# Performance work log

Measured on AMD Instinct MI355X. Metric: run time of the kernel, lower is better.

The kernel has to match this reference:

```python
import jax, jax.numpy as jnp
import numpy as np

MAX_CLUSTERS = 5
CLUSTER_SIZE_MAX = 3
K_HOP = 2
TAU = 1.0  # epoch=0 -> tau_init * decay^0 = 1.0
NEG = -1e9


def _logits(x, ctx, W1, b1, W2, b2):
    # x: [B,N,D], ctx: [B,H] -> logits [B,N] (selection_mlp, dropout=eval/identity)
    B, N, _ = x.shape
    h = jnp.concatenate([x, jnp.broadcast_to(ctx[:, None, :], (B, N, ctx.shape[-1]))], axis=-1)
    h = jax.nn.relu(h @ W1.T + b1)
    return (h @ W2.T + b2)[..., 0]


def _select(logits, cand, key):
    # Hard Gumbel-Softmax argmax over candidate nodes; zeros row if no candidates.
    any_c = cand.any(axis=-1, keepdims=True)
    ml = jnp.where(cand, logits, NEG)
    u = jax.random.uniform(key, logits.shape, dtype=logits.dtype)
    g = -jnp.log(-jnp.log(u + 1e-8) + 1e-8)
    idx = jnp.argmax((ml + g) / TAU, axis=-1)
    oh = jax.nn.one_hot(idx, logits.shape[-1], dtype=logits.dtype)
    return oh * any_c.astype(logits.dtype)


def _gru(seq, h0, Wih, Whh, bih, bhh):
    # torch nn.GRU single layer, batch_first; seq: [B,T,D], h0: [B,H] -> final hidden [B,H]
    def cell(h, xt):
        gi = xt @ Wih.T + bih
        gh = h @ Whh.T + bhh
        ir, iz, inn = jnp.split(gi, 3, axis=-1)
        hr, hz, hn = jnp.split(gh, 3, axis=-1)
        r = jax.nn.sigmoid(ir + hr)
        z = jax.nn.sigmoid(iz + hz)
        n = jnp.tanh(inn + r * hn)
        return (1.0 - z) * n + z * h, None
    h, _ = jax.lax.scan(cell, h0, jnp.swapaxes(seq, 0, 1))
    return h


def reference(x, adj, mask, W1, b1, W2, b2, Wc, bc, Wih, Whh, bih, bhh):
    B, N, D = x.shape
    key = jax.random.key(42)
    avail = mask.astype(bool)
    ctx = x.mean(axis=1) @ Wc.T + bc          # context_init  [B,H]
    h_gru = jnp.zeros_like(ctx)               # context_hidden
    assign = jnp.zeros((B, N, MAX_CLUSTERS), x.dtype)
    embs, hist = [], []
    for c in range(MAX_CLUSTERS):
        # logits are identical for every selection within this cluster (same x, same context)
        logits = _logits(x, ctx, W1, b1, W2, b2)  # [B,N]
        # seed selection (torch uses .item() -> selection is a constant index; no grad path)
        seed = jax.lax.stop_gradient(_select(logits, avail, jax.random.fold_in(key, 2 * c)))
        avail = avail & ~(seed > 0.5)
        # k-hop BFS from seed via adjacency matvecs
        reach = seed > 0.5
        cur = seed
        for _ in range(K_HOP):
            nb = jnp.einsum('bn,bnm->bm', cur, adj) > 0
            new = nb & ~reach
            reach = reach | nb
            cur = new.astype(x.dtype)
        member = seed
        for a in range(CLUSTER_SIZE_MAX - 1):
            cand = avail & reach
            sel = jax.lax.stop_gradient(_select(logits, cand, jax.random.fold_in(key, 2 * c + 1000 + a)))
            avail = avail & ~(sel > 0.5)
            member = member + sel
        assign = assign.at[:, :, c].set(member)
        cnt = member.sum(axis=-1, keepdims=True)
        emb = jnp.einsum('bn,bnd->bd', member, x) / jnp.maximum(cnt, 1.0)  # mean of member feats; 0 if empty
        embs.append(emb)
        hist.append(emb)
        # torch re-runs the GRU over the FULL cluster history each iteration, starting
        # from the previously updated hidden state (faithful to the original code)
        h_gru = _gru(jnp.stack(hist, axis=1), h_gru, Wih, Whh, bih, bhh)
        ctx = h_gru
    cluster_features = jnp.stack(embs, axis=1)               # [B,S,D]
    S = MAX_CLUSTERS
    cluster_adj = jnp.ones((B, S, S), x.dtype) - jnp.eye(S, dtype=x.dtype)[None]
    return cluster_features, cluster_adj, assign


def setup_inputs() -> dict:
    key = jax.random.key(0)
    ks = jax.random.split(key, 10)
    B, N, D, H = 16, 2048, 128, 64
    x = jax.random.normal(ks[0], (B, N, D), dtype=jnp.float32)
    # sparse symmetric binary adjacency, ~16 neighbors per node
    a = (jax.random.uniform(ks[1], (B, N, N)) < 0.004).astype(jnp.float32)
    adj = jnp.clip(a + jnp.swapaxes(a, 1, 2), 0.0, 1.0)
    adj = adj * (1.0 - jnp.eye(N, dtype=jnp.float32)[None])
    mask = jnp.ones((B, N), dtype=jnp.int32)
    s = 0.05
    return {
        'x': x, 'adj': adj, 'mask': mask,
        'W1': jax.random.normal(ks[2], (H, D + H)) * s, 'b1': jnp.zeros((H,)),
        'W2': jax.random.normal(ks[3], (1, H)) * s, 'b2': jnp.zeros((1,)),
        'Wc': jax.random.normal(ks[4], (H, D)) * s, 'bc': jnp.zeros((H,)),
        'Wih': jax.random.normal(ks[5], (3 * H, D)) * s,
        'Whh': jax.random.normal(ks[6], (3 * H, H)) * s,
        'bih': jnp.zeros((3 * H,)), 'bhh': jnp.zeros((3 * H,)),
    }
```

## Files before the change

### kernel.cpp

```cpp
#include <hip/hip_runtime.h>
#include <cfloat>
#include <cmath>

#define NB 2048
#define BB 16
#define DD 128
#define HH 64
#define MAXC 5
#define CSMAX 3
#define NT 1024

__device__ __forceinline__ unsigned rotl32(unsigned v, int d) {
  return (v << d) | (v >> (32 - d));
}

__device__ __forceinline__ void tf2x32(unsigned k0, unsigned k1, unsigned x0, unsigned x1,
                                       unsigned& o0, unsigned& o1) {
  unsigned ks2 = k0 ^ k1 ^ 0x1BD11BDAu;
  x0 += k0; x1 += k1;
#define RND(r) { x0 += x1; x1 = rotl32(x1, r); x1 ^= x0; }
  RND(13) RND(15) RND(26) RND(6)   x0 += k1;  x1 += ks2 + 1u;
  RND(17) RND(29) RND(16) RND(24)  x0 += ks2; x1 += k0 + 2u;
  RND(13) RND(15) RND(26) RND(6)   x0 += k0;  x1 += k1 + 3u;
  RND(17) RND(29) RND(16) RND(24)  x0 += k1;  x1 += ks2 + 4u;
  RND(13) RND(15) RND(26) RND(6)   x0 += ks2; x1 += k0 + 5u;
#undef RND
  o0 = x0; o1 = x1;
}

__device__ __forceinline__ float gumbel_for(unsigned k0, unsigned k1, unsigned idx) {
  unsigned o0, o1;
  tf2x32(k0, k1, 0u, idx, o0, o1);
  unsigned bits = o0 ^ o1;
  float u = __uint_as_float((bits >> 9) | 0x3f800000u) - 1.0f;
  float uu = u + 1e-8f;
  return -logf(-logf(uu) + 1e-8f);
}

__global__ __launch_bounds__(NT) void gvp_prep(
    const float* __restrict__ x, const float* __restrict__ W1,
    float* __restrict__ P, float* __restrict__ partial, float* __restrict__ gumb) {
  __shared__ __align__(16) float s_W1[HH][DD + 4];
  __shared__ float sp[8][DD];
  const int bid = blockIdx.x, tid = threadIdx.x;

  if (bid < 128) {
    for (int i = tid; i < HH * (DD / 4); i += NT) {
      int r = i >> 5, q = i & 31;
      *(float4*)&s_W1[r][q * 4] = *(const float4*)(W1 + (size_t)r * (DD + HH) + q * 4);
    }
    __syncthreads();
    const int jg = tid & 15, ng = tid >> 4;
    const int j0 = jg * 4;
    const size_t n0 = (size_t)bid * 256 + ng * 4;
    const float4* x4 = (const float4*)x;
    float acc[4][4];
#pragma unroll
    for (int i = 0; i < 4; i++)
#pragma unroll
      for (int q = 0; q < 4; q++) acc[i][q] = 0.f;
    for (int kq = 0; kq < 32; kq++) {
      float4 xv[4], wv[4];
#pragma unroll
      for (int i = 0; i < 4; i++) xv[i] = x4[(n0 + i) * 32 + kq];
#pragma unroll
      for (int q = 0; q < 4; q++) wv[q] = *(const float4*)&s_W1[j0 + q][kq * 4];
#pragma unroll
      for (int i = 0; i < 4; i++)
#pragma unroll
        for (int q = 0; q < 4; q++)
          acc[i][q] += xv[i].x * wv[q].x + xv[i].y * wv[q].y +
                       xv[i].z * wv[q].z + xv[i].w * wv[q].w;
    }
#pragma unroll
    for (int i = 0; i < 4; i++)
#pragma unroll
      for (int q = 0; q < 4; q++)
        P[(n0 + i) * HH + j0 + q] = acc[i][q];
  } else if (bid < 384) {
    const int bm = bid - 128;
    const int b = bm >> 4, chunk = bm & 15;
    const int d = tid & (DD - 1), part = tid >> 7;
    float acc = 0.f;
    const int base = chunk * 128 + part;
#pragma unroll
    for (int k = 0; k < 16; k++)
      acc += x[((size_t)b * NB + base + k * 8) * DD + d];
    sp[part][d] = acc;
    __syncthreads();
    if (tid < DD) {
      float m = 0.f;
#pragma unroll
      for (int p = 0; p < 8; p++) m += sp[p][tid];
      partial[((size_t)b * 16 + chunk) * DD + tid] = m;
    }
  } else {
    const int bg = bid - 384;
    const int base = (bg * NT + tid) * 4;
#pragma unroll
    for (int i = 0; i < 4; i++) {
      int idx = base + i;
      int sel = idx >> 15;
      int rem = idx & 32767;
      int c = sel / 3, s = sel - 3 * c;
      unsigned data = (s == 0) ? (unsigned)(2 * c) : (unsigned)(2 * c + 1000 + (s - 1));
      unsigned k0, k1;
      tf2x32(0u, 42u, 0u, data, k0, k1);
      gumb[idx] = gumbel_for(k0, k1, (unsigned)rem);
    }
  }
}

__global__ __launch_bounds__(NT, 4) void gvp_main(
    const float* __restrict__ x, const float* __restrict__ adj, const int* __restrict__ mask,
    const float* __restrict__ W1, const float* __restrict__ b1,
    const float* __restrict__ W2, const float* __restrict__ b2,
    const float* __restrict__ Wc, const float* __restrict__ bc,
    const float* __restrict__ Wih, const float* __restrict__ Whh,
    const float* __restrict__ bih, const float* __restrict__ bhh,
    const float* __restrict__ P, const float* __restrict__ partial,
    const float* __restrict__ gumb,
    float* __restrict__ out_feat, float* __restrict__ out_adjm, float* __restrict__ out_assign) {
  const int b = blockIdx.x;
  const int tid = threadIdx.x;

  __shared__ __align__(16) float s_logits[NB];
  __shared__ __align__(16) float s_gumb[2][NB];
  __shared__ unsigned char s_avail[NB], s_reach[NB], s_assignB[NB];
  __shared__ short s_list[128];
  __shared__ int s_cnt;
  __shared__ unsigned long long s_key[CSMAX];
  __shared__ __align__(16) float s_ctx[HH], s_q[HH];
  __shared__ __align__(16) float s_h[2][HH];
  __shared__ __align__(16) float s_hist[MAXC][DD];
  __shared__ __align__(16) float s_giAll[MAXC][3 * HH];
  __shared__ __align__(16) float s_Whh[3 * HH][HH + 4];
  __shared__ __align__(16) float s_W1c[HH][HH + 4];
  __shared__ __align__(16) float s_W2[HH];
  __shared__ float s_bhh[3 * HH], s_b1[HH];
  __shared__ __align__(16) float s_mean[DD];
  __shared__ float s_b2v;

  const size_t xb = (size_t)b * NB * DD;
  const float4* adj4 = (const float4*)(adj + (size_t)b * NB * NB);
  const float4* P4 = (const float4*)(P + (size_t)b * NB * HH);

  auto scanReduce = [&](float bv, int bi, int slot) {
#pragma unroll
    for (int off = 32; off; off >>= 1) {
      float ov = __shfl_down(bv, off);
      int oi = __shfl_down(bi, off);
      if (ov > bv || (ov == bv && oi < bi)) { bv = ov; bi = oi; }
    }
    if ((tid & 63) == 0 && bi < NB) {
      unsigned u = __float_as_uint(bv);
      u = (u & 0x80000000u) ? ~u : (u | 0x80000000u);
      unsigned long long key = ((unsigned long long)u << 32) | (unsigned)(~bi);
      atomicMax(&s_key[slot], key);
    }
  };
  auto decodeIdx = [](unsigned long long k) -> int {
    return k ? (int)(unsigned)(~(unsigned)k) : -1;
  };

  for (int i = tid; i < 3 * HH * (HH / 4); i += NT) {
    int r = i >> 4, q = i & 15;
    *(float4*)&s_Whh[r][q * 4] = *(const float4*)(Whh + (size_t)r * HH + q * 4);
  }
  {
    int r = tid >> 4, q = tid & 15;
    *(float4*)&s_W1c[r][q * 4] = *(const float4*)(W1 + (size_t)r * (DD + HH) + DD + q * 4);
  }
  if (tid < 3 * HH) s_bhh[tid] = bhh[tid];
  if (tid < HH) { s_W2[tid] = W2[tid]; s_b1[tid] = b1[tid]; s_h[0][tid] = 0.f; }
  if (tid == 0) s_b2v = b2[0];
#pragma unroll
  for (int r = 0; r < 2; r++) {
    int n = tid + r * NT;
    s_avail[n] = (mask[b * NB + n] != 0) ? 1 : 0;
    s_assignB[n] = 0;
  }
  if (tid < DD) {
    float m = 0.f;
#pragma unroll
    for (int k = 0; k < 16; k++) m += partial[((size_t)b * 16 + k) * DD + tid];
    s_mean[tid] = m * (1.0f / NB);
  }
  __syncthreads();
  if (tid < 4 * HH) {
    int row = tid >> 2, g = tid & 3;
    const float4* wr = (const float4*)(Wc + (size_t)row * DD) + g * 8;
    const float4* m4 = (const float4*)s_mean + g * 8;
    float s = 0.f;
#pragma unroll
    for (int i = 0; i < 8; i++) {
      float4 w = wr[i], m = m4[i];
      s += w.x * m.x + w.y * m.y + w.z * m.z + w.w * m.w;
    }
    s += __shfl_xor(s, 1);
    s += __shfl_xor(s, 2);
    if (g == 0) s_ctx[row] = s + bc[row];
  }
  __syncthreads();

  int hp = 0;

  for (int c = 0; c < MAXC; c++) {
    const float* g0p = gumb + ((size_t)(c * 3) * BB + b) * NB;
    const float4* g12 = (const float4*)(gumb + ((size_t)(c * 3 + 1 + (tid >> 9)) * BB + b) * NB);
    float4 gst = g12[tid & 511];
    const int n0 = tid, n1 = tid + NT;
    float gs0 = g0p[n0], gs1 = g0p[n1];
    ((float4*)s_gumb)[tid] = gst;
    if (tid < 4 * HH) {
      int row = tid >> 2, g = tid & 3;
      const float4* wr = (const float4*)&s_W1c[row][0] + g * 4;
      const float4* c4 = (const float4*)s_ctx + g * 4;
      float s = 0.f;
#pragma unroll
      for (int i = 0; i < 4; i++) {
        float4 w = wr[i], cc = c4[i];
        s += w.x * cc.x + w.y * cc.y + w.z * cc.z + w.w * cc.w;
      }
      s += __shfl_xor(s, 1);
      s += __shfl_xor(s, 2);
      if (g == 0) s_q[row] = s + s_b1[row];
    }
    if (tid < CSMAX) s_key[tid] = 0ull;
    if (tid == 0) s_cnt = 0;
    __syncthreads();

    {
      float l0 = s_b2v, l1 = s_b2v;
      const float4* p0 = P4 + (size_t)n0 * 16;
      const float4* p1 = P4 + (size_t)n1 * 16;
      const float4* q4 = (const float4*)s_q;
      const float4* w4 = (const float4*)s_W2;
#pragma unroll
      for (int qq = 0; qq < 16; qq += 4) {
        float4 A[4], Bv[4];
#pragma unroll
        for (int i = 0; i < 4; i++) { A[i] = p0[qq + i]; Bv[i] = p1[qq + i]; }
#pragma unroll
        for (int i = 0; i < 4; i++) {
          float4 qv = q4[qq + i], w = w4[qq + i];
          l0 += w.x * fmaxf(A[i].x + qv.x, 0.f) + w.y * fmaxf(A[i].y + qv.y, 0.f) +
                w.z * fmaxf(A[i].z + qv.z, 0.f) + w.w * fmaxf(A[i].w + qv.w, 0.f);
          l1 += w.x * fmaxf(Bv[i].x + qv.x, 0.f) + w.y * fmaxf(Bv[i].y + qv.y, 0.f) +
                w.z * fmaxf(Bv[i].z + qv.z, 0.f) + w.w * fmaxf(Bv[i].w + qv.w, 0.f);
        }
      }
      s_logits[n0] = l0;
      s_logits[n1] = l1;
      float bv = -FLT_MAX;
      int bi = NB;
      if (s_avail[n0]) { float y = l0 + gs0; if (y > bv) { bv = y; bi = n0; } }
      if (s_avail[n1]) { float y = l1 + gs1; if (y > bv || (y == bv && n1 < bi)) { bv = y; bi = n1; } }
      scanReduce(bv, bi, 0);
    }
    __syncthreads();

    const int seed = decodeIdx(s_key[0]);
    if (tid < 512) {
      if (seed >= 0) {
        float4 a = adj4[(size_t)seed * 512 + tid];
        int m = tid << 2;
        unsigned f0 = a.x > 0.f, f1 = a.y > 0.f, f2 = a.z > 0.f, f3 = a.w > 0.f;
        unsigned r = f0 | (f1 << 8) | (f2 << 16) | (f3 << 24);
        if ((seed >> 2) == tid) r |= 1u << ((seed & 3) * 8);
        ((unsigned*)s_reach)[tid] = r;
        if (f0 && m != seed)     { int p = atomicAdd(&s_cnt, 1); if (p < 128) s_list[p] = (short)m; }
        if (f1 && m + 1 != seed) { int p = atomicAdd(&s_cnt, 1); if (p < 128) s_list[p] = (short)(m + 1); }
        if (f2 && m + 2 != seed) { int p = atomicAdd(&s_cnt, 1); if (p < 128) s_list[p] = (short)(m + 2); }
        if (f3 && m + 3 != seed) { int p = atomicAdd(&s_cnt, 1); if (p < 128) s_list[p] = (short)(m + 3); }
      } else {
        ((unsigned*)s_reach)[tid] = 0u;
      }
    }
    __syncthreads();

    if (seed >= 0) {
      int cnt = min(s_cnt, 128);
      int m4 = tid & 511, rg = tid >> 9;
      bool a0 = false, a1 = false, a2 = false, a3 = false;
#pragma unroll
      for (int k = 0; k < 20; k++) {
        int li = rg + 2 * k;
        if (li < cnt) {
          int n = s_list[li];
          float4 a = adj4[(size_t)n * 512 + m4];
          a0 |= a.x > 0.f; a1 |= a.y > 0.f; a2 |= a.z > 0.f; a3 |= a.w > 0.f;
        }
      }
      for (int li = rg + 40; li < cnt; li += 2) {
        int n = s_list[li];
        float4 a = adj4[(size_t)n * 512 + m4];
        a0 |= a.x > 0.f; a1 |= a.y > 0.f; a2 |= a.z > 0.f; a3 |= a.w > 0.f;
      }
      int m = m4 << 2;
      if (a0) s_reach[m] = 1;
      if (a1) s_reach[m + 1] = 1;
      if (a2) s_reach[m + 2] = 1;
      if (a3) s_reach[m + 3] = 1;
    }
    __syncthreads();

    {
      float bv = -FLT_MAX;
      int bi = NB;
#pragma unroll
      for (int r = 0; r < 2; r++) {
        int n = tid + r * NT;
        if (s_avail[n] && s_reach[n] && n != seed) {
          float y = s_logits[n] + s_gumb[0][n];
          if (y > bv || (y == bv && n < bi)) { bv = y; bi = n; }
        }
      }
      scanReduce(bv, bi, 1);
    }
    __syncthreads();

    const int w1i = decodeIdx(s_key[1]);
    {
      float bv = -FLT_MAX;
      int bi = NB;
#pragma unroll
      for (int r = 0; r < 2; r++) {
        int n = tid + r * NT;
        if (s_avail[n] && s_reach[n] && n != seed && n != w1i) {
          float y = s_logits[n] + s_gumb[1][n];
          if (y > bv || (y == bv && n < bi)) { bv = y; bi = n; }
        }
      }
      scanReduce(bv, bi, 2);
    }
    __syncthreads();

    const int w2i = decodeIdx(s_key[2]);
    {
      int mc = (seed >= 0) + (w1i >= 0) + (w2i >= 0);
      if (tid < DD) {
        float acc = 0.f;
        if (seed >= 0) acc += x[xb + (size_t)seed * DD + tid];
        if (w1i >= 0) acc += x[xb + (size_t)w1i * DD + tid];
        if (w2i >= 0) acc += x[xb + (size_t)w2i * DD + tid];
        float e = acc / fmaxf((float)mc, 1.0f);
        s_hist[c][tid] = e;
        out_feat[((size_t)b * MAXC + c) * DD + tid] = e;
      } else if (tid >= 128 && tid < 128 + CSMAX) {
        int idx = (tid == 128) ? seed : (tid == 129 ? w1i : w2i);
        if (idx >= 0) { s_avail[idx] = 0; s_assignB[idx] |= (unsigned char)(1 << c); }
      }
    }
    __syncthreads();

    if (tid < 4 * 3 * HH) {
      int row = tid >> 2, g = tid & 3;
      const float4* wr = (const float4*)(Wih + (size_t)row * DD) + g * 8;
      const float4* h4 = (const float4*)s_hist[c] + g * 8;
      float s = 0.f;
#pragma unroll
      for (int i = 0; i < 8; i++) {
        float4 w = wr[i], hh = h4[i];
        s += w.x * hh.x + w.y * hh.y + w.z * hh.z + w.w * hh.w;
      }
      s += __shfl_xor(s, 1);
      s += __shfl_xor(s, 2);
      if (g == 0) s_giAll[c][row] = s + bih[row];
    }
    __syncthreads();

    for (int t0 = 0; t0 <= c; t0++) {
      if (tid < 4 * HH) {
        int row = tid >> 2, g = tid & 3;
        const float4* h4 = (const float4*)s_h[hp] + g * 4;
        float4 hv[4];
#pragma unroll
        for (int i = 0; i < 4; i++) hv[i] = h4[i];
        const float4* wr = (const float4*)&s_Whh[row][0] + g * 4;
        const float4* wz = (const float4*)&s_Whh[HH + row][0] + g * 4;
        const float4* wn = (const float4*)&s_Whh[2 * HH + row][0] + g * 4;
        float sr = 0.f, sz = 0.f, sn = 0.f;
#pragma unroll
        for (int i = 0; i < 4; i++) {
          float4 a = wr[i], bz = wz[i], cn = wn[i], h = hv[i];
          sr += a.x * h.x + a.y * h.y + a.z * h.z + a.w * h.w;
          sz += bz.x * h.x + bz.y * h.y + bz.z * h.z + bz.w * h.w;
          sn += cn.x * h.x + cn.y * h.y + cn.z * h.z + cn.w * h.w;
        }
        sr += __shfl_xor(sr, 1); sr += __shfl_xor(sr, 2);
        sz += __shfl_xor(sz, 1); sz += __shfl_xor(sz, 2);
        sn += __shfl_xor(sn, 1); sn += __shfl_xor(sn, 2);
        if (g == 0) {
          float r = 1.f / (1.f + expf(-(s_giAll[t0][row] + sr + s_bhh[row])));
          float z = 1.f / (1.f + expf(-(s_giAll[t0][HH + row] + sz + s_bhh[HH + row])));
          float nn = tanhf(s_giAll[t0][2 * HH + row] + r * (sn + s_bhh[2 * HH + row]));
          float hn = (1.f - z) * nn + z * s_h[hp][row];
          s_h[hp ^ 1][row] = hn;
          if (t0 == c) s_ctx[row] = hn;
        }
      }
      hp ^= 1;
      __syncthreads();
    }
  }

#pragma unroll
  for (int r = 0; r < 2; r++) {
    int n = tid + r * NT;
    unsigned bits = s_assignB[n];
    size_t base = ((size_t)(b * NB + n)) * MAXC;
#pragma unroll
    for (int cc = 0; cc < MAXC; cc++)
      out_assign[base + cc] = (float)((bits >> cc) & 1u);
  }
  for (int i = tid; i < MAXC * MAXC; i += NT)
    out_adjm[(size_t)b * MAXC * MAXC + i] = ((i / MAXC) == (i % MAXC)) ? 0.f : 1.f;
}

extern "C" void kernel_launch(void* const* d_in, const int* in_sizes, int n_in,
                              void* d_out, int out_size, void* d_ws, size_t ws_size,
                              hipStream_t stream) {
  const float* x   = (const float*)d_in[0];
  const float* adj = (const float*)d_in[1];
  const int*   mask= (const int*)d_in[2];
  const float* W1  = (const float*)d_in[3];
  const float* b1  = (const float*)d_in[4];
  const float* W2  = (const float*)d_in[5];
  const float* b2  = (const float*)d_in[6];
  const float* Wc  = (const float*)d_in[7];
  const float* bc  = (const float*)d_in[8];
  const float* Wih = (const float*)d_in[9];
  const float* Whh = (const float*)d_in[10];
  const float* bih = (const float*)d_in[11];
  const float* bhh = (const float*)d_in[12];

  float* ws = (float*)d_ws;
  float* P       = ws;
  float* partial = P + (size_t)BB * NB * HH;
  float* gumb    = partial + (size_t)BB * 16 * DD;

  float* out = (float*)d_out;
  float* out_feat = out;
  float* out_adjm = out + (size_t)BB * MAXC * DD;
  float* out_assign = out_adjm + (size_t)BB * MAXC * MAXC;

  hipLaunchKernelGGL(gvp_prep, dim3(504), dim3(NT), 0, stream, x, W1, P, partial, gumb);
  hipLaunchKernelGGL(gvp_main, dim3(BB), dim3(NT), 0, stream,
                     x, adj, mask, W1, b1, W2, b2, Wc, bc, Wih, Whh, bih, bhh, P, partial, gumb,
                     out_feat, out_adjm, out_assign);
}
```

Baseline: 195.0 us.

## Split monolithic per-batch kernel into per-cluster launches with inline Gumbel noise

Replaces the single persistent 16-block main kernel with a chain of small kernels per cluster: logits plus seed selection, BFS plus a joint top-2 pick of both members, a GRU update, and a final assignment writer. Gumbel noise is now computed inline instead of being precomputed into a large buffer, and the two sequential member argmaxes are merged into one top-2 reduction. State is passed between launches through workspace. This adds about 16 launches, each still using only 16 blocks, and moves state through global memory, trading launch overhead for less serialized work inside one block.

```diff
diff --git a/kernel.cpp b/kernel.cpp
--- a/kernel.cpp
+++ b/kernel.cpp
@@ -7,8 +7,15 @@
 #define DD 128
 #define HH 64
 #define MAXC 5
-#define CSMAX 3
 #define NT 1024
+
+#define OFF_P 0
+#define OFF_PARTIAL (OFF_P + BB * NB * HH)
+#define OFF_LOGITS OFF_PARTIAL
+#define OFF_QV (OFF_PARTIAL + BB * 16 * DD)
+#define OFF_HRUN (OFF_QV + BB * HH)
+#define OFF_GI (OFF_HRUN + BB * HH)
+#define OFF_WIN (OFF_GI + BB * MAXC * 3 * HH)
 
 __device__ __forceinline__ unsigned rotl32(unsigned v, int d) {
   return (v << d) | (v >> (32 - d));
@@ -37,12 +44,22 @@
   return -logf(-logf(uu) + 1e-8f);
 }
 
+__device__ __forceinline__ unsigned long long packKey(float y, int n) {
+  unsigned u = __float_as_uint(y);
+  u = (u & 0x80000000u) ? ~u : (u | 0x80000000u);
+  return ((unsigned long long)u << 32) | (unsigned)(~(unsigned)n);
+}
+__device__ __forceinline__ int decodeKey(unsigned long long k) {
+  return k ? (int)(~(unsigned)k) : -1;
+}
+
 __global__ __launch_bounds__(NT) void gvp_prep(
-    const float* __restrict__ x, const float* __restrict__ W1,
-    float* __restrict__ P, float* __restrict__ partial, float* __restrict__ gumb) {
+    const float* __restrict__ x, const float* __restrict__ W1, float* __restrict__ ws) {
   __shared__ __align__(16) float s_W1[HH][DD + 4];
   __shared__ float sp[8][DD];
   const int bid = blockIdx.x, tid = threadIdx.x;
+  float* P = ws + OFF_P;
+  float* partial = ws + OFF_PARTIAL;
 
   if (bid < 128) {
     for (int i = tid; i < HH * (DD / 4); i += NT) {
@@ -77,7 +94,7 @@
 #pragma unroll
       for (int q = 0; q < 4; q++)
         P[(n0 + i) * HH + j0 + q] = acc[i][q];
-  } else if (bid < 384) {
+  } else {
     const int bm = bid - 128;
     const int b = bm >> 4, chunk = bm & 15;
     const int d = tid & (DD - 1), part = tid >> 7;
@@ -94,328 +111,372 @@
       for (int p = 0; p < 8; p++) m += sp[p][tid];
       partial[((size_t)b * 16 + chunk) * DD + tid] = m;
     }
-  } else {
-    const int bg = bid - 384;
-    const int base = (bg * NT + tid) * 4;
+  }
+}
+
+__global__ __launch_bounds__(256) void gvp_init(
+    const float* __restrict__ Wc, const float* __restrict__ bc,
+    const float* __restrict__ W1, const float* __restrict__ b1, float* __restrict__ ws) {
+  __shared__ __align__(16) float s_mean[DD], s_ctx[HH];
+  __shared__ __align__(16) float s_W1c[HH][HH + 4];
+  const int b = blockIdx.x, tid = threadIdx.x;
+  for (int i = tid; i < HH * 16; i += 256) {
+    int r = i >> 4, q = i & 15;
+    *(float4*)&s_W1c[r][q * 4] = *(const float4*)(W1 + (size_t)r * (DD + HH) + DD + q * 4);
+  }
+  if (tid < DD) {
+    float m = 0.f;
+#pragma unroll
+    for (int k = 0; k < 16; k++) m += ws[OFF_PARTIAL + ((size_t)b * 16 + k) * DD + tid];
+    s_mean[tid] = m * (1.0f / NB);
+  }
+  __syncthreads();
+  {
+    int row = tid >> 2, g = tid & 3;
+    const float4* wr = (const float4*)(Wc + (size_t)row * DD) + g * 8;
+    const float4* m4 = (const float4*)s_mean + g * 8;
+    float s = 0.f;
+#pragma unroll
+    for (int i = 0; i < 8; i++) {
+      float4 w = wr[i], m = m4[i];
+      s += w.x * m.x + w.y * m.y + w.z * m.z + w.w * m.w;
+    }
+    s += __shfl_xor(s, 1);
+    s += __shfl_xor(s, 2);
+    if (g == 0) s_ctx[row] = s + bc[row];
+  }
+  __syncthreads();
+  {
+    int row = tid >> 2, g = tid & 3;
+    const float4* wr = (const float4*)&s_W1c[row][0] + g * 4;
+    const float4* c4 = (const float4*)s_ctx + g * 4;
+    float s = 0.f;
 #pragma unroll
     for (int i = 0; i < 4; i++) {
-      int idx = base + i;
-      int sel = idx >> 15;
-      int rem = idx & 32767;
-      int c = sel / 3, s = sel - 3 * c;
-      unsigned data = (s == 0) ? (unsigned)(2 * c) : (unsigned)(2 * c + 1000 + (s - 1));
-      unsigned k0, k1;
-      tf2x32(0u, 42u, 0u, data, k0, k1);
-      gumb[idx] = gumbel_for(k0, k1, (unsigned)rem);
-    }
-  }
-}
-
-__global__ __launch_bounds__(NT, 4) void gvp_main(
+      float4 w = wr[i], cc = c4[i];
+      s += w.x * cc.x + w.y * cc.y + w.z * cc.z + w.w * cc.w;
+    }
+    s += __shfl_xor(s, 1);
+    s += __shfl_xor(s, 2);
+    if (g == 0) ws[OFF_QV + b * HH + row] = s + b1[row];
+  }
+  if (tid < HH) ws[OFF_HRUN + b * HH + tid] = 0.f;
+}
+
+__global__ __launch_bounds__(NT) void gvp_selA(
+    const int* __restrict__ mask, const float* __restrict__ W2, const float* __restrict__ b2,
+    float* __restrict__ ws, int c) {
+  __shared__ __align__(16) float s_q[HH], s_W2[HH];
+  __shared__ int s_win[16];
+  __shared__ unsigned long long s_key0;
+  const int b = blockIdx.x, tid = threadIdx.x;
+  const int n0 = tid, n1 = tid + NT;
+  int* winners = (int*)(ws + OFF_WIN) + b * 16;
+
+  if (tid == 0) s_key0 = 0ull;
+  if (tid < HH) s_q[tid] = ws[OFF_QV + b * HH + tid];
+  else if (tid < 2 * HH) s_W2[tid - HH] = W2[tid - HH];
+  else if (tid < 2 * HH + 16) {
+    int i = tid - 2 * HH;
+    s_win[i] = (i < 3 * c) ? winners[i] : -1;
+  }
+  __syncthreads();
+
+  const float4* P4 = (const float4*)(ws + OFF_P) + (size_t)b * NB * 16;
+  const float4* q4 = (const float4*)s_q;
+  const float4* w4 = (const float4*)s_W2;
+  const float4* p0 = P4 + (size_t)n0 * 16;
+  const float4* p1 = P4 + (size_t)n1 * 16;
+  float l0 = b2[0], l1 = l0;
+#pragma unroll
+  for (int i = 0; i < 16; i++) {
+    float4 pa = p0[i], pb = p1[i], qv = q4[i], w = w4[i];
+    l0 += w.x * fmaxf(pa.x + qv.x, 0.f) + w.y * fmaxf(pa.y + qv.y, 0.f) +
+          w.z * fmaxf(pa.z + qv.z, 0.f) + w.w * fmaxf(pa.w + qv.w, 0.f);
+    l1 += w.x * fmaxf(pb.x + qv.x, 0.f) + w.y * fmaxf(pb.y + qv.y, 0.f) +
+          w.z * fmaxf(pb.z + qv.z, 0.f) + w.w * fmaxf(pb.w + qv.w, 0.f);
+  }
+  ws[OFF_LOGITS + (size_t)b * NB + n0] = l0;
+  ws[OFF_LOGITS + (size_t)b * NB + n1] = l1;
+
+  unsigned k0, k1;
+  tf2x32(0u, 42u, 0u, (unsigned)(2 * c), k0, k1);
+  bool a0 = mask[b * NB + n0] != 0, a1 = mask[b * NB + n1] != 0;
+  for (int i = 0; i < 3 * c; i++) {
+    int w = s_win[i];
+    a0 &= (n0 != w);
+    a1 &= (n1 != w);
+  }
+  float bv = -FLT_MAX;
+  int bi = NB;
+  if (a0) { float y = l0 + gumbel_for(k0, k1, (unsigned)(b * NB + n0)); if (y > bv) { bv = y; bi = n0; } }
+  if (a1) { float y = l1 + gumbel_for(k0, k1, (unsigned)(b * NB + n1)); if (y > bv) { bv = y; bi = n1; } }
+#pragma unroll
+  for (int off = 32; off; off >>= 1) {
+    float ov = __shfl_down(bv, off);
+    int oi = __shfl_down(bi, off);
+    if (ov > bv || (ov == bv && oi < bi)) { bv = ov; bi = oi; }
+  }
+  if ((tid & 63) == 0 && bi < NB) atomicMax(&s_key0, packKey(bv, bi));
+  __syncthreads();
+  if (tid == 0) winners[3 * c] = decodeKey(s_key0);
+}
+
+__global__ __launch_bounds__(NT) void gvp_selB(
     const float* __restrict__ x, const float* __restrict__ adj, const int* __restrict__ mask,
-    const float* __restrict__ W1, const float* __restrict__ b1,
-    const float* __restrict__ W2, const float* __restrict__ b2,
-    const float* __restrict__ Wc, const float* __restrict__ bc,
-    const float* __restrict__ Wih, const float* __restrict__ Whh,
-    const float* __restrict__ bih, const float* __restrict__ bhh,
-    const float* __restrict__ P, const float* __restrict__ partial,
-    const float* __restrict__ gumb,
-    float* __restrict__ out_feat, float* __restrict__ out_adjm, float* __restrict__ out_assign) {
-  const int b = blockIdx.x;
-  const int tid = threadIdx.x;
-
+    const float* __restrict__ Wih, const float* __restrict__ bih,
+    float* __restrict__ ws, float* __restrict__ out_feat, int c) {
   __shared__ __align__(16) float s_logits[NB];
-  __shared__ __align__(16) float s_gumb[2][NB];
-  __shared__ unsigned char s_avail[NB], s_reach[NB], s_assignB[NB];
+  __shared__ unsigned char s_avail[NB], s_reach[NB];
   __shared__ short s_list[128];
   __shared__ int s_cnt;
-  __shared__ unsigned long long s_key[CSMAX];
-  __shared__ __align__(16) float s_ctx[HH], s_q[HH];
-  __shared__ __align__(16) float s_h[2][HH];
-  __shared__ __align__(16) float s_hist[MAXC][DD];
-  __shared__ __align__(16) float s_giAll[MAXC][3 * HH];
-  __shared__ __align__(16) float s_Whh[3 * HH][HH + 4];
-  __shared__ __align__(16) float s_W1c[HH][HH + 4];
-  __shared__ __align__(16) float s_W2[HH];
-  __shared__ float s_bhh[3 * HH], s_b1[HH];
-  __shared__ __align__(16) float s_mean[DD];
-  __shared__ float s_b2v;
-
+  __shared__ unsigned long long s_key1;
+  __shared__ unsigned long long s_top2[16][2];
+  __shared__ int s_win[16];
+  const int b = blockIdx.x, tid = threadIdx.x, wid = tid >> 6;
+  const int n0 = tid, n1 = tid + NT;
+  int* winners = (int*)(ws + OFF_WIN) + b * 16;
+  const float4* adj4 = (const float4*)(adj + (size_t)b * NB * NB);
   const size_t xb = (size_t)b * NB * DD;
-  const float4* adj4 = (const float4*)(adj + (size_t)b * NB * NB);
-  const float4* P4 = (const float4*)(P + (size_t)b * NB * HH);
-
-  auto scanReduce = [&](float bv, int bi, int slot) {
+
+  if (tid == 0) { s_cnt = 0; s_key1 = 0ull; }
+  if (tid >= 32 && tid < 64) s_top2[(tid - 32) >> 1][(tid - 32) & 1] = 0ull;
+  if (tid >= 64 && tid < 80) {
+    int i = tid - 64;
+    s_win[i] = (i <= 3 * c) ? winners[i] : -1;
+  }
+  s_logits[n0] = ws[OFF_LOGITS + (size_t)b * NB + n0];
+  s_logits[n1] = ws[OFF_LOGITS + (size_t)b * NB + n1];
+  s_avail[n0] = (mask[b * NB + n0] != 0) ? 1 : 0;
+  s_avail[n1] = (mask[b * NB + n1] != 0) ? 1 : 0;
+  __syncthreads();
+
+  const int seed = s_win[3 * c];
+  if (tid < 512) {
+    if (seed >= 0) {
+      float4 a = adj4[(size_t)seed * 512 + tid];
+      int m = tid << 2;
+      unsigned f0 = a.x > 0.f, f1 = a.y > 0.f, f2 = a.z > 0.f, f3 = a.w > 0.f;
+      unsigned r = f0 | (f1 << 8) | (f2 << 16) | (f3 << 24);
+      if ((seed >> 2) == tid) r |= 1u << ((seed & 3) * 8);
+      ((unsigned*)s_reach)[tid] = r;
+      if (f0 && m != seed)     { int p = atomicAdd(&s_cnt, 1); if (p < 128) s_list[p] = (short)m; }
+      if (f1 && m + 1 != seed) { int p = atomicAdd(&s_cnt, 1); if (p < 128) s_list[p] = (short)(m + 1); }
+      if (f2 && m + 2 != seed) { int p = atomicAdd(&s_cnt, 1); if (p < 128) s_list[p] = (short)(m + 2); }
+      if (f3 && m + 3 != seed) { int p = atomicAdd(&s_cnt, 1); if (p < 128) s_list[p] = (short)(m + 3); }
+    } else {
+      ((unsigned*)s_reach)[tid] = 0u;
+    }
+  }
+  unsigned k10, k11, k20, k21;
+  tf2x32(0u, 42u, 0u, (unsigned)(2 * c + 1000), k10, k11);
+  tf2x32(0u, 42u, 0u, (unsigned)(2 * c + 1001), k20, k21);
+  float g1a = gumbel_for(k10, k11, (unsigned)(b * NB + n0));
+  float g1b = gumbel_for(k10, k11, (unsigned)(b * NB + n1));
+  float g2a = gumbel_for(k20, k21, (unsigned)(b * NB + n0));
+  float g2b = gumbel_for(k20, k21, (unsigned)(b * NB + n1));
+  __syncthreads();
+
+  if (seed >= 0) {
+    int cnt = min(s_cnt, 128);
+    int m4 = tid & 511, rg = tid >> 9;
+    bool a0 = false, a1 = false, a2 = false, a3 = false;
+#pragma unroll
+    for (int k = 0; k < 20; k++) {
+      int li = rg + 2 * k;
+      if (li < cnt) {
+        int n = s_list[li];
+        float4 a = adj4[(size_t)n * 512 + m4];
+        a0 |= a.x > 0.f; a1 |= a.y > 0.f; a2 |= a.z > 0.f; a3 |= a.w > 0.f;
+      }
+    }
+    for (int li = rg + 40; li < cnt; li += 2) {
+      int n = s_list[li];
+      float4 a = adj4[(size_t)n * 512 + m4];
+      a0 |= a.x > 0.f; a1 |= a.y > 0.f; a2 |= a.z > 0.f; a3 |= a.w > 0.f;
+    }
+    int m = m4 << 2;
+    if (a0) s_reach[m] = 1;
+    if (a1) s_reach[m + 1] = 1;
+    if (a2) s_reach[m + 2] = 1;
+    if (a3) s_reach[m + 3] = 1;
+  }
+  __syncthreads();
+
+  {
+    bool c0 = s_avail[n0] && s_reach[n0];
+    bool c1 = s_avail[n1] && s_reach[n1];
+    for (int i = 0; i <= 3 * c; i++) {
+      int w = s_win[i];
+      c0 &= (n0 != w);
+      c1 &= (n1 != w);
+    }
+    float bv = -FLT_MAX;
+    int bi = NB;
+    if (c0) { float y = s_logits[n0] + g1a; if (y > bv) { bv = y; bi = n0; } }
+    if (c1) { float y = s_logits[n1] + g1b; if (y > bv || (y == bv && n1 < bi)) { bv = y; bi = n1; } }
+    unsigned long long ka = c0 ? packKey(s_logits[n0] + g2a, n0) : 0ull;
+    unsigned long long kb = c1 ? packKey(s_logits[n1] + g2b, n1) : 0ull;
+    unsigned long long t1 = ka > kb ? ka : kb, t2 = ka > kb ? kb : ka;
 #pragma unroll
     for (int off = 32; off; off >>= 1) {
       float ov = __shfl_down(bv, off);
       int oi = __shfl_down(bi, off);
       if (ov > bv || (ov == bv && oi < bi)) { bv = ov; bi = oi; }
-    }
-    if ((tid & 63) == 0 && bi < NB) {
-      unsigned u = __float_as_uint(bv);
-      u = (u & 0x80000000u) ? ~u : (u | 0x80000000u);
-      unsigned long long key = ((unsigned long long)u << 32) | (unsigned)(~bi);
-      atomicMax(&s_key[slot], key);
-    }
-  };
-  auto decodeIdx = [](unsigned long long k) -> int {
-    return k ? (int)(unsigned)(~(unsigned)k) : -1;
-  };
-
-  for (int i = tid; i < 3 * HH * (HH / 4); i += NT) {
-    int r = i >> 4, q = i & 15;
-    *(float4*)&s_Whh[r][q * 4] = *(const float4*)(Whh + (size_t)r * HH + q * 4);
-  }
+      unsigned long long o1 = __shfl_down(t1, off);
+      unsigned long long o2 = __shfl_down(t2, off);
+      unsigned long long lo = t1 < o1 ? t1 : o1;
+      unsigned long long hi2 = t2 > o2 ? t2 : o2;
+      t1 = t1 > o1 ? t1 : o1;
+      t2 = lo > hi2 ? lo : hi2;
+    }
+    if ((tid & 63) == 0) {
+      if (bi < NB) atomicMax(&s_key1, packKey(bv, bi));
+      s_top2[wid][0] = t1;
+      s_top2[wid][1] = t2;
+    }
+  }
+  __syncthreads();
+
   {
-    int r = tid >> 4, q = tid & 15;
-    *(float4*)&s_W1c[r][q * 4] = *(const float4*)(W1 + (size_t)r * (DD + HH) + DD + q * 4);
-  }
-  if (tid < 3 * HH) s_bhh[tid] = bhh[tid];
-  if (tid < HH) { s_W2[tid] = W2[tid]; s_b1[tid] = b1[tid]; s_h[0][tid] = 0.f; }
-  if (tid == 0) s_b2v = b2[0];
-#pragma unroll
-  for (int r = 0; r < 2; r++) {
-    int n = tid + r * NT;
-    s_avail[n] = (mask[b * NB + n] != 0) ? 1 : 0;
-    s_assignB[n] = 0;
-  }
-  if (tid < DD) {
-    float m = 0.f;
-#pragma unroll
-    for (int k = 0; k < 16; k++) m += partial[((size_t)b * 16 + k) * DD + tid];
-    s_mean[tid] = m * (1.0f / NB);
-  }
-  __syncthreads();
-  if (tid < 4 * HH) {
-    int row = tid >> 2, g = tid & 3;
-    const float4* wr = (const float4*)(Wc + (size_t)row * DD) + g * 8;
-    const float4* m4 = (const float4*)s_mean + g * 8;
-    float s = 0.f;
-#pragma unroll
-    for (int i = 0; i < 8; i++) {
-      float4 w = wr[i], m = m4[i];
-      s += w.x * m.x + w.y * m.y + w.z * m.z + w.w * m.w;
-    }
-    s += __shfl_xor(s, 1);
-    s += __shfl_xor(s, 2);
-    if (g == 0) s_ctx[row] = s + bc[row];
-  }
-  __syncthreads();
-
-  int hp = 0;
-
-  for (int c = 0; c < MAXC; c++) {
-    const float* g0p = gumb + ((size_t)(c * 3) * BB + b) * NB;
-    const float4* g12 = (const float4*)(gumb + ((size_t)(c * 3 + 1 + (tid >> 9)) * BB + b) * NB);
-    float4 gst = g12[tid & 511];
-    const int n0 = tid, n1 = tid + NT;
-    float gs0 = g0p[n0], gs1 = g0p[n1];
-    ((float4*)s_gumb)[tid] = gst;
-    if (tid < 4 * HH) {
+    int w1 = decodeKey(s_key1);
+    unsigned long long t1 = 0ull, t2 = 0ull;
+#pragma unroll
+    for (int i = 0; i < 16; i++) {
+      unsigned long long k = s_top2[i][0];
+      if (k > t1) { t2 = t1; t1 = k; } else if (k > t2) t2 = k;
+      k = s_top2[i][1];
+      if (k > t1) { t2 = t1; t1 = k; } else if (k > t2) t2 = k;
+    }
+    int i1 = decodeKey(t1);
+    int w2 = (i1 == w1) ? decodeKey(t2) : i1;
+    int mc = (seed >= 0) + (w1 >= 0) + (w2 >= 0);
+    float invmc = 1.0f / fmaxf((float)mc, 1.0f);
+
+    if (tid < 768) {
       int row = tid >> 2, g = tid & 3;
-      const float4* wr = (const float4*)&s_W1c[row][0] + g * 4;
-      const float4* c4 = (const float4*)s_ctx + g * 4;
+      const float4* wr = (const float4*)(Wih + (size_t)row * DD) + g * 8;
+      const float4* x0 = (seed >= 0) ? (const float4*)(x + xb + (size_t)seed * DD) + g * 8 : nullptr;
+      const float4* x1 = (w1 >= 0) ? (const float4*)(x + xb + (size_t)w1 * DD) + g * 8 : nullptr;
+      const float4* x2 = (w2 >= 0) ? (const float4*)(x + xb + (size_t)w2 * DD) + g * 8 : nullptr;
       float s = 0.f;
 #pragma unroll
-      for (int i = 0; i < 4; i++) {
-        float4 w = wr[i], cc = c4[i];
-        s += w.x * cc.x + w.y * cc.y + w.z * cc.z + w.w * cc.w;
+      for (int i = 0; i < 8; i++) {
+        float4 w = wr[i];
+        float sx = 0.f, sy = 0.f, sz = 0.f, sw = 0.f;
+        if (x0) { float4 v = x0[i]; sx += v.x; sy += v.y; sz += v.z; sw += v.w; }
+        if (x1) { float4 v = x1[i]; sx += v.x; sy += v.y; sz += v.z; sw += v.w; }
+        if (x2) { float4 v = x2[i]; sx += v.x; sy += v.y; sz += v.z; sw += v.w; }
+        s += w.x * sx + w.y * sy + w.z * sz + w.w * sw;
       }
       s += __shfl_xor(s, 1);
       s += __shfl_xor(s, 2);
-      if (g == 0) s_q[row] = s + s_b1[row];
-    }
-    if (tid < CSMAX) s_key[tid] = 0ull;
-    if (tid == 0) s_cnt = 0;
+      if (g == 0) ws[OFF_GI + ((size_t)b * MAXC + c) * 3 * HH + row] = s * invmc + bih[row];
+    } else if (tid < 768 + DD) {
+      int d = tid - 768;
+      float acc = 0.f;
+      if (seed >= 0) acc += x[xb + (size_t)seed * DD + d];
+      if (w1 >= 0) acc += x[xb + (size_t)w1 * DD + d];
+      if (w2 >= 0) acc += x[xb + (size_t)w2 * DD + d];
+      out_feat[((size_t)b * MAXC + c) * DD + d] = acc * invmc;
+    } else if (tid == 896) winners[3 * c + 1] = w1;
+    else if (tid == 897) winners[3 * c + 2] = w2;
+  }
+}
+
+__global__ __launch_bounds__(256) void gvp_gru(
+    const float* __restrict__ Whh, const float* __restrict__ bhh,
+    const float* __restrict__ W1, const float* __restrict__ b1,
+    float* __restrict__ ws, int c) {
+  __shared__ __align__(16) float s_Whh[3 * HH][HH + 4];
+  __shared__ __align__(16) float s_W1c[HH][HH + 4];
+  __shared__ __align__(16) float s_gi[MAXC][3 * HH];
+  __shared__ __align__(16) float s_h[2][HH];
+  __shared__ float s_bhh[3 * HH];
+  const int b = blockIdx.x, tid = threadIdx.x;
+
+  for (int i = tid; i < 3 * HH * 16; i += 256) {
+    int r = i >> 4, q = i & 15;
+    *(float4*)&s_Whh[r][q * 4] = *(const float4*)(Whh + (size_t)r * HH + q * 4);
+  }
+  for (int i = tid; i < HH * 16; i += 256) {
+    int r = i >> 4, q = i & 15;
+    *(float4*)&s_W1c[r][q * 4] = *(const float4*)(W1 + (size_t)r * (DD + HH) + DD + q * 4);
+  }
+  if (tid < 3 * HH) {
+    s_bhh[tid] = bhh[tid];
+    for (int t = 0; t <= c; t++)
+      s_gi[t][tid] = ws[OFF_GI + ((size_t)b * MAXC + t) * 3 * HH + tid];
+  }
+  if (tid < HH) s_h[0][tid] = ws[OFF_HRUN + b * HH + tid];
+  __syncthreads();
+
+  int hp = 0;
+  for (int t = 0; t <= c; t++) {
+    int row = tid >> 2, g = tid & 3;
+    const float4* h4 = (const float4*)s_h[hp] + g * 4;
+    float4 hv[4];
+#pragma unroll
+    for (int i = 0; i < 4; i++) hv[i] = h4[i];
+    const float4* wr = (const float4*)&s_Whh[row][0] + g * 4;
+    const float4* wz = (const float4*)&s_Whh[HH + row][0] + g * 4;
+    const float4* wn = (const float4*)&s_Whh[2 * HH + row][0] + g * 4;
+    float sr = 0.f, sz = 0.f, sn = 0.f;
+#pragma unroll
+    for (int i = 0; i < 4; i++) {
+      float4 a = wr[i], bz = wz[i], cn = wn[i], h = hv[i];
+      sr += a.x * h.x + a.y * h.y + a.z * h.z + a.w * h.w;
+      sz += bz.x * h.x + bz.y * h.y + bz.z * h.z + bz.w * h.w;
+      sn += cn.x * h.x + cn.y * h.y + cn.z * h.z + cn.w * h.w;
+    }
+    sr += __shfl_xor(sr, 1); sr += __shfl_xor(sr, 2);
+    sz += __shfl_xor(sz, 1); sz += __shfl_xor(sz, 2);
+    sn += __shfl_xor(sn, 1); sn += __shfl_xor(sn, 2);
+    if (g == 0) {
+      float r = 1.f / (1.f + expf(-(s_gi[t][row] + sr + s_bhh[row])));
+      float z = 1.f / (1.f + expf(-(s_gi[t][HH + row] + sz + s_bhh[HH + row])));
+      float nn = tanhf(s_gi[t][2 * HH + row] + r * (sn + s_bhh[2 * HH + row]));
+      s_h[hp ^ 1][row] = (1.f - z) * nn + z * s_h[hp][row];
+    }
+    hp ^= 1;
     __syncthreads();
-
-    {
-      float l0 = s_b2v, l1 = s_b2v;
-      const float4* p0 = P4 + (size_t)n0 * 16;
-      const float4* p1 = P4 + (size_t)n1 * 16;
-      const float4* q4 = (const float4*)s_q;
-      const float4* w4 = (const float4*)s_W2;
-#pragma unroll
-      for (int qq = 0; qq < 16; qq += 4) {
-        float4 A[4], Bv[4];
-#pragma unroll
-        for (int i = 0; i < 4; i++) { A[i] = p0[qq + i]; Bv[i] = p1[qq + i]; }
-#pragma unroll
-        for (int i = 0; i < 4; i++) {
-          float4 qv = q4[qq + i], w = w4[qq + i];
-          l0 += w.x * fmaxf(A[i].x + qv.x, 0.f) + w.y * fmaxf(A[i].y + qv.y, 0.f) +
-                w.z * fmaxf(A[i].z + qv.z, 0.f) + w.w * fmaxf(A[i].w + qv.w, 0.f);
-          l1 += w.x * fmaxf(Bv[i].x + qv.x, 0.f) + w.y * fmaxf(Bv[i].y + qv.y, 0.f) +
-                w.z * fmaxf(Bv[i].z + qv.z, 0.f) + w.w * fmaxf(Bv[i].w + qv.w, 0.f);
-        }
-      }
-      s_logits[n0] = l0;
-      s_logits[n1] = l1;
-      float bv = -FLT_MAX;
-      int bi = NB;
-      if (s_avail[n0]) { float y = l0 + gs0; if (y > bv) { bv = y; bi = n0; } }
-      if (s_avail[n1]) { float y = l1 + gs1; if (y > bv || (y == bv && n1 < bi)) { bv = y; bi = n1; } }
-      scanReduce(bv, bi, 0);
-    }
+  }
+  {
+    int row = tid >> 2, g = tid & 3;
+    const float4* wr = (const float4*)&s_W1c[row][0] + g * 4;
+    const float4* c4 = (const float4*)s_h[hp] + g * 4;
+    float s = 0.f;
+#pragma unroll
+    for (int i = 0; i < 4; i++) {
+      float4 w = wr[i], cc = c4[i];
+      s += w.x * cc.x + w.y * cc.y + w.z * cc.z + w.w * cc.w;
+    }
+    s += __shfl_xor(s, 1);
+    s += __shfl_xor(s, 2);
+    if (g == 0) ws[OFF_QV + b * HH + row] = s + b1[row];
+  }
+  if (tid < HH) ws[OFF_HRUN + b * HH + tid] = s_h[hp][tid];
+}
+
+__global__ __launch_bounds__(NT) void gvp_final(
+    const float* __restrict__ ws, float* __restrict__ out_adjm, float* __restrict__ out_assign) {
+  __shared__ int s_win[16];
+  const int tid = threadIdx.x;
+  if (blockIdx.x < 160) {
+    int b = blockIdx.x / 10;
+    const int* winners = (const int*)(ws + OFF_WIN) + b * 16;
+    if (tid < 16) s_win[tid] = (tid < 15) ? winners[tid] : -1;
     __syncthreads();
-
-    const int seed = decodeIdx(s_key[0]);
-    if (tid < 512) {
-      if (seed >= 0) {
-        float4 a = adj4[(size_t)seed * 512 + tid];
-        int m = tid << 2;
-        unsigned f0 = a.x > 0.f, f1 = a.y > 0.f, f2 = a.z > 0.f, f3 = a.w > 0.f;
-        unsigned r = f0 | (f1 << 8) | (f2 << 16) | (f3 << 24);
-        if ((seed >> 2) == tid) r |= 1u << ((seed & 3) * 8);
-        ((unsigned*)s_reach)[tid] = r;
-        if (f0 && m != seed)     { int p = atomicAdd(&s_cnt, 1); if (p < 128) s_list[p] = (short)m; }
-        if (f1 && m + 1 != seed) { int p = atomicAdd(&s_cnt, 1); if (p < 128) s_list[p] = (short)(m + 1); }
-        if (f2 && m + 2 != seed) { int p = atomicAdd(&s_cnt, 1); if (p < 128) s_list[p] = (short)(m + 2); }
-        if (f3 && m + 3 != seed) { int p = atomicAdd(&s_cnt, 1); if (p < 128) s_list[p] = (short)(m + 3); }
-      } else {
-        ((unsigned*)s_reach)[tid] = 0u;
-      }
-    }
-    __syncthreads();
-
-    if (seed >= 0) {
-      int cnt = min(s_cnt, 128);
-      int m4 = tid & 511, rg = tid >> 9;
-      bool a0 = false, a1 = false, a2 = false, a3 = false;
-#pragma unroll
-      for (int k = 0; k < 20; k++) {
-        int li = rg + 2 * k;
-        if (li < cnt) {
-          int n = s_list[li];
-          float4 a = adj4[(size_t)n * 512 + m4];
-          a0 |= a.x > 0.f; a1 |= a.y > 0.f; a2 |= a.z > 0.f; a3 |= a.w > 0.f;
-        }
-      }
-      for (int li = rg + 40; li < cnt; li += 2) {
-        int n = s_list[li];
-        float4 a = adj4[(size_t)n * 512 + m4];
-        a0 |= a.x > 0.f; a1 |= a.y > 0.f; a2 |= a.z > 0.f; a3 |= a.w > 0.f;
-      }
-      int m = m4 << 2;
-      if (a0) s_reach[m] = 1;
-      if (a1) s_reach[m + 1] = 1;
-      if (a2) s_reach[m + 2] = 1;
-      if (a3) s_reach[m + 3] = 1;
-    }
-    __syncthreads();
-
-    {
-      float bv = -FLT_MAX;
-      int bi = NB;
-#pragma unroll
-      for (int r = 0; r < 2; r++) {
-        int n = tid + r * NT;
-        if (s_avail[n] && s_reach[n] && n != seed) {
-          float y = s_logits[n] + s_gumb[0][n];
-          if (y > bv || (y == bv && n < bi)) { bv = y; bi = n; }
-        }
-      }
-      scanReduce(bv, bi, 1);
-    }
-    __syncthreads();
-
-    const int w1i = decodeIdx(s_key[1]);
-    {
-      float bv = -FLT_MAX;
-      int bi = NB;
-#pragma unroll
-      for (int r = 0; r < 2; r++) {
-        int n = tid + r * NT;
-        if (s_avail[n] && s_reach[n] && n != seed && n != w1i) {
-          float y = s_logits[n] + s_gumb[1][n];
-          if (y > bv || (y == bv && n < bi)) { bv = y; bi = n; }
-        }
-      }
-      scanReduce(bv, bi, 2);
-    }
-    __syncthreads();
-
-    const int w2i = decodeIdx(s_key[2]);
-    {
-      int mc = (seed >= 0) + (w1i >= 0) + (w2i >= 0);
-      if (tid < DD) {
-        float acc = 0.f;
-        if (seed >= 0) acc += x[xb + (size_t)seed * DD + tid];
-        if (w1i >= 0) acc += x[xb + (size_t)w1i * DD + tid];
-        if (w2i >= 0) acc += x[xb + (size_t)w2i * DD + tid];
-        float e = acc / fmaxf((float)mc, 1.0f);
-        s_hist[c][tid] = e;
-        out_feat[((size_t)b * MAXC + c) * DD + tid] = e;
-      } else if (tid >= 128 && tid < 128 + CSMAX) {
-        int idx = (tid == 128) ? seed : (tid == 129 ? w1i : w2i);
-        if (idx >= 0) { s_avail[idx] = 0; s_assignB[idx] |= (unsigned char)(1 << c); }
-      }
-    }
-    __syncthreads();
-
-    if (tid < 4 * 3 * HH) {
-      int row = tid >> 2, g = tid & 3;
-      const float4* wr = (const float4*)(Wih + (size_t)row * DD) + g * 8;
-      const float4* h4 = (const float4*)s_hist[c] + g * 8;
-      float s = 0.f;
-#pragma unroll
-      for (int i = 0; i < 8; i++) {
-        float4 w = wr[i], hh = h4[i];
-        s += w.x * hh.x + w.y * hh.y + w.z * hh.z + w.w * hh.w;
-      }
-      s += __shfl_xor(s, 1);
-      s += __shfl_xor(s, 2);
-      if (g == 0) s_giAll[c][row] = s + bih[row];
-    }
-    __syncthreads();
-
-    for (int t0 = 0; t0 <= c; t0++) {
-      if (tid < 4 * HH) {
-        int row = tid >> 2, g = tid & 3;
-        const float4* h4 = (const float4*)s_h[hp] + g * 4;
-        float4 hv[4];
-#pragma unroll
-        for (int i = 0; i < 4; i++) hv[i] = h4[i];
-        const float4* wr = (const float4*)&s_Whh[row][0] + g * 4;
-        const float4* wz = (const float4*)&s_Whh[HH + row][0] + g * 4;
-        const float4* wn = (const float4*)&s_Whh[2 * HH + row][0] + g * 4;
-        float sr = 0.f, sz = 0.f, sn = 0.f;
-#pragma unroll
-        for (int i = 0; i < 4; i++) {
-          float4 a = wr[i], bz = wz[i], cn = wn[i], h = hv[i];
-          sr += a.x * h.x + a.y * h.y + a.z * h.z + a.w * h.w;
-          sz += bz.x * h.x + bz.y * h.y + bz.z * h.z + bz.w * h.w;
-          sn += cn.x * h.x + cn.y * h.y + cn.z * h.z + cn.w * h.w;
-        }
-        sr += __shfl_xor(sr, 1); sr += __shfl_xor(sr, 2);
-        sz += __shfl_xor(sz, 1); sz += __shfl_xor(sz, 2);
-        sn += __shfl_xor(sn, 1); sn += __shfl_xor(sn, 2);
-        if (g == 0) {
-          float r = 1.f / (1.f + expf(-(s_giAll[t0][row] + sr + s_bhh[row])));
-          float z = 1.f / (1.f + expf(-(s_giAll[t0][HH + row] + sz + s_bhh[HH + row])));
-          float nn = tanhf(s_giAll[t0][2 * HH + row] + r * (sn + s_bhh[2 * HH + row]));
-          float hn = (1.f - z) * nn + z * s_h[hp][row];
-          s_h[hp ^ 1][row] = hn;
-          if (t0 == c) s_ctx[row] = hn;
-        }
-      }
-      hp ^= 1;
-      __syncthreads();
-    }
-  }
-
-#pragma unroll
-  for (int r = 0; r < 2; r++) {
-    int n = tid + r * NT;
-    unsigned bits = s_assignB[n];
-    size_t base = ((size_t)(b * NB + n)) * MAXC;
-#pragma unroll
-    for (int cc = 0; cc < MAXC; cc++)
-      out_assign[base + cc] = (float)((bits >> cc) & 1u);
-  }
-  for (int i = tid; i < MAXC * MAXC; i += NT)
-    out_adjm[(size_t)b * MAXC * MAXC + i] = ((i / MAXC) == (i % MAXC)) ? 0.f : 1.f;
+    int r = (blockIdx.x % 10) * NT + tid;
+    int n = r / 5, cc = r - 5 * n;
+    int m0 = s_win[3 * cc], m1 = s_win[3 * cc + 1], m2 = s_win[3 * cc + 2];
+    out_assign[(size_t)b * (NB * MAXC) + r] = (n == m0 || n == m1 || n == m2) ? 1.0f : 0.0f;
+  } else {
+    if (tid < BB * MAXC * MAXC) {
+      int i = tid % (MAXC * MAXC);
+      out_adjm[tid] = ((i / MAXC) == (i % MAXC)) ? 0.f : 1.f;
+    }
+  }
 }
 
 extern "C" void kernel_launch(void* const* d_in, const int* in_sizes, int n_in,
@@ -436,17 +497,19 @@
   const float* bhh = (const float*)d_in[12];
 
   float* ws = (float*)d_ws;
-  float* P       = ws;
-  float* partial = P + (size_t)BB * NB * HH;
-  float* gumb    = partial + (size_t)BB * 16 * DD;
-
   float* out = (float*)d_out;
   float* out_feat = out;
   float* out_adjm = out + (size_t)BB * MAXC * DD;
   float* out_assign = out_adjm + (size_t)BB * MAXC * MAXC;
 
-  hipLaunchKernelGGL(gvp_prep, dim3(504), dim3(NT), 0, stream, x, W1, P, partial, gumb);
-  hipLaunchKernelGGL(gvp_main, dim3(BB), dim3(NT), 0, stream,
-                     x, adj, mask, W1, b1, W2, b2, Wc, bc, Wih, Whh, bih, bhh, P, partial, gumb,
-                     out_feat, out_adjm, out_assign);
-}
+  hipLaunchKernelGGL(gvp_prep, dim3(384), dim3(NT), 0, stream, x, W1, ws);
+  hipLaunchKernelGGL(gvp_init, dim3(BB), dim3(256), 0, stream, Wc, bc, W1, b1, ws);
+  for (int c = 0; c < MAXC; c++) {
+    hipLaunchKernelGGL(gvp_selA, dim3(BB), dim3(NT), 0, stream, mask, W2, b2, ws, c);
+    hipLaunchKernelGGL(gvp_selB, dim3(BB), dim3(NT), 0, stream,
+                       x, adj, mask, Wih, bih, ws, out_feat, c);
+    if (c + 1 < MAXC)
+      hipLaunchKernelGGL(gvp_gru, dim3(BB), dim3(256), 0, stream, Whh, bhh, W1, b1, ws, c);
+  }
+  hipLaunchKernelGGL(gvp_final, dim3(161), dim3(NT), 0, stream, ws, out_adjm, out_assign);
+}
```

Result: slower. 282.7 us (+45.0%).
